# Kernel tuning notes

Hardware: AMD Instinct MI355X
Metric: run time of the kernel (lower is better)

Reference implementation:

```python
import jax, jax.numpy as jnp
import numpy as np

PS = 32
EMBED_DIM = 768
IN_CH = 3
IMG = 1024
NUM_PATCHES = 992  # ini_row = i for H=1024, so need i+32 <= 1024
SPIKE_IDX = np.array([5, 300, 800])
SPIKE_VAL = 1.0e6  # makes val ~= 23.94 < 24 -> nearest size 16 -> subdivided


def _token_layout(iw_np, num_patches, ps, H):
    """Replicates the module's data-dependent patch-size / subpatch-position logic.
    Returns static (rows, cols, sizes) for every output token, in emission order."""
    avg = iw_np.mean()
    val = np.minimum(ps * avg ** 0.05 / iw_np ** 0.05, float(ps))
    choices = np.array([32, 16, 8, 4], dtype=np.float64)  # argmin picks first on tie, like min(list)
    sizes = choices[np.argmin(np.abs(val[:, None] - choices[None, :]), axis=1)].astype(np.int64)
    rows, cols, szs = [], [], []
    for i in range(num_patches):
        ini_col = (i * ps) % H
        ini_row = (i * ps * ps) // H
        s = int(sizes[i])
        if 3 < s < ps:
            ns = ps // s  # num_subpatches; subpatch_size == s
            for j in range(ns):
                rows.append(ini_row + (j * s) // ns)
                cols.append(ini_col + (j * s) % (ns * s))
                szs.append(s)
        else:
            rows.append(ini_row)
            cols.append(ini_col)
            szs.append(ps)
    return np.asarray(rows), np.asarray(cols), np.asarray(szs)


def _embed(x, W, b, rows, cols, szs, ps):
    E, C = W.shape[0], W.shape[1]
    B = x.shape[0]
    T = szs.shape[0]
    out = jnp.zeros((B, T, E), dtype=x.dtype)
    for s in np.unique(szs):
        s = int(s)
        idx = np.nonzero(szs == s)[0]  # static token slots for this size group
        r, c = rows[idx], cols[idx]
        if s == ps:
            Wf = W
        else:
            kd = ps // s  # fold the ps x ps kernel down to s x s, as in the module
            Wf = W.reshape(E, C, kd, kd, s, s).sum(axis=(2, 3))
        ar = np.arange(s)
        # gather [B, C, K, s, s] sub-patches with static advanced indexing
        patches = x[:, :, r[:, None, None] + ar[None, :, None], c[:, None, None] + ar[None, None, :]]
        tok = jnp.einsum('bckhw,echw->bke', patches, Wf) + b  # stride==kernel -> 1 token each
        out = out.at[:, jnp.asarray(idx), :].set(tok)
    return out


def setup_inputs() -> dict:
    key = jax.random.key(0)
    k_x, k_w, k_iw, k_b = jax.random.split(key, 4)
    x = jax.random.normal(k_x, (8, IN_CH, IMG, IMG), dtype=jnp.float32)
    iw = jax.random.uniform(k_iw, (1, NUM_PATCHES), dtype=jnp.float32, minval=0.5, maxval=1.5)
    iw = iw.at[0, SPIKE_IDX].set(SPIKE_VAL)  # 3 high-importance patches -> size-16 subdivision
    W = jax.random.normal(k_w, (EMBED_DIM, IN_CH, PS, PS), dtype=jnp.float32) * 0.02
    b = jax.random.normal(k_b, (EMBED_DIM,), dtype=jnp.float32) * 0.02
    return {"x": x, "importance_weights": iw, "W": W, "b": b, "num_patches": NUM_PATCHES}


def reference(x, importance_weights, W, b, num_patches):
    iw = np.asarray(importance_weights)[0]
    rows, cols, szs = _token_layout(iw, int(num_patches), PS, x.shape[3])
    return _embed(x, W, b, rows, cols, szs, PS)  # [B, T, E]
```

## Files before the change

### kernel.cpp

```cpp
#include <hip/hip_runtime.h>


typedef __attribute__((ext_vector_type(8))) short bf16x8;
typedef __attribute__((ext_vector_type(4))) float f32x4;

#define K_DIM 3072
#define N_DIM 768
#define KSPLIT 2

__device__ __forceinline__ unsigned short f2bf(float f) {
  unsigned int u = __float_as_uint(f);
  u += 0x7fffu + ((u >> 16) & 1u);
  return (unsigned short)(u >> 16);
}

__device__ __forceinline__ void gload16(const void* g, void* l) {
  __builtin_amdgcn_global_load_lds(
      (const __attribute__((address_space(1))) void*)g,
      (__attribute__((address_space(3))) void*)l, 16, 0, 0);
}

__global__ __launch_bounds__(1024)
void prep_kernel(const float* __restrict__ W, unsigned short* __restrict__ Wb, int w4,
                 const float* __restrict__ bias, float* __restrict__ out, int out4,
                 const float* __restrict__ iw, int P,
                 int* __restrict__ tokBase, int* __restrict__ tokMask,
                 int NB_W, int NB_BIAS) {
  int bid = blockIdx.x;
  int tid = threadIdx.x;
  if (bid < NB_W) {
    int idx = bid * 1024 + tid;
    if (idx < w4) {
      float4 f = *(const float4*)(W + (size_t)idx * 4);
      ushort4 o;
      o.x = f2bf(f.x); o.y = f2bf(f.y); o.z = f2bf(f.z); o.w = f2bf(f.w);
      *(ushort4*)(Wb + (size_t)idx * 4) = o;
    }
    return;
  }
  if (bid < NB_W + NB_BIAS) {
    int idx = (bid - NB_W) * 1024 + tid;
    if (idx < out4) {
      int n = (idx % (N_DIM / 4)) * 4;
      *(float4*)(out + (size_t)idx * 4) = *(const float4*)(bias + n);
    }
    return;
  }
  __shared__ double s_wsum[16];
  __shared__ double s_avg;
  __shared__ int s_cnt[1024];
  float v = (tid < P) ? iw[tid] : 0.0f;
  double d = (double)v;
#pragma unroll
  for (int off = 32; off > 0; off >>= 1) d += __shfl_down(d, off, 64);
  if ((tid & 63) == 0) s_wsum[tid >> 6] = d;
  __syncthreads();
  if (tid == 0) {
    double s = 0.0;
    for (int i = 0; i < 16; ++i) s += s_wsum[i];
    s_avg = s / (double)P;
  }
  __syncthreads();
  int cnt = 0, sz = 32;
  if (tid < P) {
    double val = 32.0 * pow(s_avg / (double)v, 0.05);
    if (val > 32.0) val = 32.0;
    sz = (val >= 24.0) ? 32 : (val >= 12.0) ? 16 : (val >= 6.0) ? 8 : 4;
    cnt = (sz < 32) ? (32 / sz) : 1;
  }
  s_cnt[tid] = cnt;
  __syncthreads();
  for (int dl = 1; dl < 1024; dl <<= 1) {
    int add = (tid >= dl) ? s_cnt[tid - dl] : 0;
    __syncthreads();
    s_cnt[tid] += add;
    __syncthreads();
  }
  if (tid < P) {
    int off = s_cnt[tid] - cnt;
    int ini_col = (tid * 32) & 1023;
    int ini_row = (tid * 32 * 32) >> 10;
    if (sz == 32) {
      tokBase[off] = ini_row * 1024 + ini_col;
      tokMask[off] = 31;
    } else {
      int ns = 32 / sz;
      for (int j = 0; j < ns; ++j) {
        int r = ini_row + (j * sz) / ns;
        int c = ini_col + ((j * sz) & 31);
        tokBase[off + j] = r * 1024 + c;
        tokMask[off + j] = sz - 1;
      }
    }
  }
}

__global__ __launch_bounds__(256)
void gather_kernel(const float* __restrict__ x,
                   const int* __restrict__ tokBase,
                   const int* __restrict__ tokMask,
                   unsigned short* __restrict__ Ab) {
  int t = blockIdx.x;
  int b = blockIdx.y;
  int T = gridDim.x;
  int m = b * T + t;
  int base = tokBase[t];
  int mask = tokMask[t];
  int sh = __popc(mask);
  const float* xb = x + (size_t)b * 3145728 + (size_t)base;
  unsigned short* arow = Ab + (size_t)m * K_DIM;
#pragma unroll
  for (int it = 0; it < 3; ++it) {
    int g = it * 256 + threadIdx.x;
    int p = g * 4;
    int c = p >> 10;
    int f = p & 1023;
    int h = (f >> sh) & mask;
    int w = f & mask;
    float4 fv = *(const float4*)(xb + (size_t)c * 1048576 + h * 1024 + w);
    ushort4 o;
    o.x = f2bf(fv.x); o.y = f2bf(fv.y); o.z = f2bf(fv.z); o.w = f2bf(fv.w);
    *(ushort4*)(arow + p) = o;
  }
}

__global__ __launch_bounds__(256, 4)
void gemm_kernel(const unsigned short* __restrict__ A, const unsigned short* __restrict__ Wb,
                 float* __restrict__ out, int Mtot) {
  __shared__ unsigned short Alds[128 * 32];
  __shared__ unsigned short Blds[128 * 32];
  int tid = threadIdx.x;
  int lane = tid & 63;
  int wave = tid >> 6;
  int wr = wave >> 1, wc = wave & 1;
  int mBase = blockIdx.y * 128;
  int nBase = blockIdx.x * 128;
  int kBase = blockIdx.z * (K_DIM / KSPLIT);

  f32x4 acc[4][4] = {};

  int sr = lane >> 2;
  int sc = lane & 3;
  const unsigned short* Ag0 = A + (size_t)(mBase + wave * 32 + sr) * K_DIM + sc * 8 + kBase;
  const unsigned short* Ag1 = Ag0 + (size_t)16 * K_DIM;
  const unsigned short* Bg0 = Wb + (size_t)(nBase + wave * 32 + sr) * K_DIM + sc * 8 + kBase;
  const unsigned short* Bg1 = Bg0 + (size_t)16 * K_DIM;
  unsigned short* Al0 = Alds + wave * 1024 + lane * 8;
  unsigned short* Al1 = Al0 + 512;
  unsigned short* Bl0 = Blds + wave * 1024 + lane * 8;
  unsigned short* Bl1 = Bl0 + 512;

  int rr = lane & 15, q = lane >> 4;

  for (int k0 = 0; k0 < K_DIM / KSPLIT; k0 += 32) {
    gload16(Ag0 + k0, Al0);
    gload16(Ag1 + k0, Al1);
    gload16(Bg0 + k0, Bl0);
    gload16(Bg1 + k0, Bl1);
    __syncthreads();

    bf16x8 aF[4], bF[4];
#pragma unroll
    for (int i = 0; i < 4; ++i)
      aF[i] = *(const bf16x8*)&Alds[(wr * 64 + i * 16 + rr) * 32 + q * 8];
#pragma unroll
    for (int j = 0; j < 4; ++j)
      bF[j] = *(const bf16x8*)&Blds[(wc * 64 + j * 16 + rr) * 32 + q * 8];
#pragma unroll
    for (int i = 0; i < 4; ++i)
#pragma unroll
      for (int j = 0; j < 4; ++j)
        acc[i][j] = __builtin_amdgcn_mfma_f32_16x16x32_bf16(aF[i], bF[j], acc[i][j], 0, 0, 0);
    __syncthreads();
  }

#pragma unroll
  for (int j = 0; j < 4; ++j) {
    int n = nBase + wc * 64 + j * 16 + rr;
#pragma unroll
    for (int i = 0; i < 4; ++i) {
      int mrow = mBase + wr * 64 + i * 16 + q * 4;
#pragma unroll
      for (int r2 = 0; r2 < 4; ++r2) {
        int m = mrow + r2;
        if (m < Mtot) atomicAdd(&out[(size_t)m * N_DIM + n], acc[i][j][r2]);
      }
    }
  }
}

extern "C" void kernel_launch(void* const* d_in, const int* in_sizes, int n_in,
                              void* d_out, int out_size, void* d_ws, size_t ws_size,
                              hipStream_t stream) {
  const float* x  = (const float*)d_in[0];
  const float* iw = (const float*)d_in[1];
  const float* W  = (const float*)d_in[2];
  const float* b  = (const float*)d_in[3];
  int P = in_sizes[1];
  int B = in_sizes[0] / (3 * 1024 * 1024);
  int E = in_sizes[3];
  int T = out_size / (B * E);
  int Mtot = B * T;
  int Mpad = (Mtot + 127) & ~127;

  char* ws = (char*)d_ws;
  int* tokBase = (int*)ws;
  int* tokMask = (int*)(ws + 32768);
  unsigned short* Wb = (unsigned short*)(ws + 65536);
  unsigned short* Ab = (unsigned short*)(ws + 65536 + (size_t)E * K_DIM * 2);

  int w4 = E * K_DIM / 4;
  int out4 = out_size / 4;
  int NB_W = (w4 + 1023) / 1024;
  int NB_BIAS = (out4 + 1023) / 1024;
  prep_kernel<<<NB_W + NB_BIAS + 1, 1024, 0, stream>>>(
      W, Wb, w4, b, (float*)d_out, out4, iw, P, tokBase, tokMask, NB_W, NB_BIAS);

  dim3 gGrid(T, B);
  gather_kernel<<<gGrid, 256, 0, stream>>>(x, tokBase, tokMask, Ab);

  dim3 grid(N_DIM / 128, Mpad / 128, KSPLIT);
  gemm_kernel<<<grid, 256, 0, stream>>>(Ab, Wb, (float*)d_out, Mtot);
}
```

Measured before the change: 262.9 us.

## Drop split-K atomics, fuse bias into GEMM epilogue, register-prefetch pipeline

Removes the split-K decomposition, so each GEMM block covers the full K range and writes its results directly with the bias added, rather than pre-filling the output with bias and accumulating with atomics. The global_load_lds path is replaced by register prefetching: the next K-slice is loaded into registers while the current slice is staged into LDS and fed to MFMA. This removes the bias-fill pass and the atomic traffic, at the cost of half as many GEMM blocks, which lowers parallelism. The launch bound is relaxed to allow more registers for the prefetch buffers.

```diff
diff --git a/kernel.cpp b/kernel.cpp
--- a/kernel.cpp
+++ b/kernel.cpp
@@ -6,7 +6,6 @@
 
 #define K_DIM 3072
 #define N_DIM 768
-#define KSPLIT 2
 
 __device__ __forceinline__ unsigned short f2bf(float f) {
   unsigned int u = __float_as_uint(f);
@@ -14,18 +13,10 @@
   return (unsigned short)(u >> 16);
 }
 
-__device__ __forceinline__ void gload16(const void* g, void* l) {
-  __builtin_amdgcn_global_load_lds(
-      (const __attribute__((address_space(1))) void*)g,
-      (__attribute__((address_space(3))) void*)l, 16, 0, 0);
-}
-
 __global__ __launch_bounds__(1024)
 void prep_kernel(const float* __restrict__ W, unsigned short* __restrict__ Wb, int w4,
-                 const float* __restrict__ bias, float* __restrict__ out, int out4,
                  const float* __restrict__ iw, int P,
-                 int* __restrict__ tokBase, int* __restrict__ tokMask,
-                 int NB_W, int NB_BIAS) {
+                 int* __restrict__ tokBase, int* __restrict__ tokMask, int NB_W) {
   int bid = blockIdx.x;
   int tid = threadIdx.x;
   if (bid < NB_W) {
@@ -35,14 +26,6 @@
       ushort4 o;
       o.x = f2bf(f.x); o.y = f2bf(f.y); o.z = f2bf(f.z); o.w = f2bf(f.w);
       *(ushort4*)(Wb + (size_t)idx * 4) = o;
-    }
-    return;
-  }
-  if (bid < NB_W + NB_BIAS) {
-    int idx = (bid - NB_W) * 1024 + tid;
-    if (idx < out4) {
-      int n = (idx % (N_DIM / 4)) * 4;
-      *(float4*)(out + (size_t)idx * 4) = *(const float4*)(bias + n);
     }
     return;
   }
@@ -124,9 +107,9 @@
   }
 }
 
-__global__ __launch_bounds__(256, 4)
+__global__ __launch_bounds__(256, 2)
 void gemm_kernel(const unsigned short* __restrict__ A, const unsigned short* __restrict__ Wb,
-                 float* __restrict__ out, int Mtot) {
+                 const float* __restrict__ bias, float* __restrict__ out, int Mtot) {
   __shared__ unsigned short Alds[128 * 32];
   __shared__ unsigned short Blds[128 * 32];
   int tid = threadIdx.x;
@@ -135,55 +118,76 @@
   int wr = wave >> 1, wc = wave & 1;
   int mBase = blockIdx.y * 128;
   int nBase = blockIdx.x * 128;
-  int kBase = blockIdx.z * (K_DIM / KSPLIT);
 
   f32x4 acc[4][4] = {};
 
-  int sr = lane >> 2;
-  int sc = lane & 3;
-  const unsigned short* Ag0 = A + (size_t)(mBase + wave * 32 + sr) * K_DIM + sc * 8 + kBase;
-  const unsigned short* Ag1 = Ag0 + (size_t)16 * K_DIM;
-  const unsigned short* Bg0 = Wb + (size_t)(nBase + wave * 32 + sr) * K_DIM + sc * 8 + kBase;
-  const unsigned short* Bg1 = Bg0 + (size_t)16 * K_DIM;
-  unsigned short* Al0 = Alds + wave * 1024 + lane * 8;
-  unsigned short* Al1 = Al0 + 512;
-  unsigned short* Bl0 = Blds + wave * 1024 + lane * 8;
-  unsigned short* Bl1 = Bl0 + 512;
+  const unsigned short* Ag0 = A + (size_t)(mBase + (tid >> 2)) * K_DIM + (tid & 3) * 8;
+  const unsigned short* Ag1 = Ag0 + (size_t)64 * K_DIM;
+  const unsigned short* Bg0 = Wb + (size_t)(nBase + (tid >> 2)) * K_DIM + (tid & 3) * 8;
+  const unsigned short* Bg1 = Bg0 + (size_t)64 * K_DIM;
+  unsigned short* Al0 = Alds + tid * 8;
+  unsigned short* Al1 = Al0 + 2048;
+  unsigned short* Bl0 = Blds + tid * 8;
+  unsigned short* Bl1 = Bl0 + 2048;
 
   int rr = lane & 15, q = lane >> 4;
 
-  for (int k0 = 0; k0 < K_DIM / KSPLIT; k0 += 32) {
-    gload16(Ag0 + k0, Al0);
-    gload16(Ag1 + k0, Al1);
-    gload16(Bg0 + k0, Bl0);
-    gload16(Bg1 + k0, Bl1);
-    __syncthreads();
-
-    bf16x8 aF[4], bF[4];
-#pragma unroll
-    for (int i = 0; i < 4; ++i)
-      aF[i] = *(const bf16x8*)&Alds[(wr * 64 + i * 16 + rr) * 32 + q * 8];
-#pragma unroll
-    for (int j = 0; j < 4; ++j)
-      bF[j] = *(const bf16x8*)&Blds[(wc * 64 + j * 16 + rr) * 32 + q * 8];
-#pragma unroll
-    for (int i = 0; i < 4; ++i)
-#pragma unroll
-      for (int j = 0; j < 4; ++j)
-        acc[i][j] = __builtin_amdgcn_mfma_f32_16x16x32_bf16(aF[i], bF[j], acc[i][j], 0, 0, 0);
-    __syncthreads();
+  int4 ra0, ra1, rb0, rb1;
+  int4 sa0, sa1, sb0, sb1;
+
+  ra0 = *(const int4*)(Ag0); ra1 = *(const int4*)(Ag1);
+  rb0 = *(const int4*)(Bg0); rb1 = *(const int4*)(Bg1);
+
+#define MFMA_STAGE()                                                        \
+  {                                                                         \
+    bf16x8 aF[4], bF[4];                                                    \
+    _Pragma("unroll")                                                       \
+    for (int i = 0; i < 4; ++i)                                             \
+      aF[i] = *(const bf16x8*)&Alds[(wr * 64 + i * 16 + rr) * 32 + q * 8];  \
+    _Pragma("unroll")                                                       \
+    for (int j = 0; j < 4; ++j)                                             \
+      bF[j] = *(const bf16x8*)&Blds[(wc * 64 + j * 16 + rr) * 32 + q * 8];  \
+    _Pragma("unroll")                                                       \
+    for (int i = 0; i < 4; ++i)                                             \
+      _Pragma("unroll")                                                     \
+      for (int j = 0; j < 4; ++j)                                           \
+        acc[i][j] = __builtin_amdgcn_mfma_f32_16x16x32_bf16(aF[i], bF[j],   \
+                                                            acc[i][j], 0, 0, 0); \
+  }
+
+  for (int k0 = 0; k0 < K_DIM; k0 += 64) {
+    if (k0 + 32 < K_DIM) {
+      sa0 = *(const int4*)(Ag0 + k0 + 32); sa1 = *(const int4*)(Ag1 + k0 + 32);
+      sb0 = *(const int4*)(Bg0 + k0 + 32); sb1 = *(const int4*)(Bg1 + k0 + 32);
+    }
+    __syncthreads();
+    *(int4*)Al0 = ra0; *(int4*)Al1 = ra1;
+    *(int4*)Bl0 = rb0; *(int4*)Bl1 = rb1;
+    __syncthreads();
+    MFMA_STAGE();
+
+    if (k0 + 64 < K_DIM) {
+      ra0 = *(const int4*)(Ag0 + k0 + 64); ra1 = *(const int4*)(Ag1 + k0 + 64);
+      rb0 = *(const int4*)(Bg0 + k0 + 64); rb1 = *(const int4*)(Bg1 + k0 + 64);
+    }
+    __syncthreads();
+    *(int4*)Al0 = sa0; *(int4*)Al1 = sa1;
+    *(int4*)Bl0 = sb0; *(int4*)Bl1 = sb1;
+    __syncthreads();
+    MFMA_STAGE();
   }
 
 #pragma unroll
   for (int j = 0; j < 4; ++j) {
     int n = nBase + wc * 64 + j * 16 + rr;
+    float bv = bias[n];
 #pragma unroll
     for (int i = 0; i < 4; ++i) {
       int mrow = mBase + wr * 64 + i * 16 + q * 4;
 #pragma unroll
       for (int r2 = 0; r2 < 4; ++r2) {
         int m = mrow + r2;
-        if (m < Mtot) atomicAdd(&out[(size_t)m * N_DIM + n], acc[i][j][r2]);
+        if (m < Mtot) out[(size_t)m * N_DIM + n] = acc[i][j][r2] + bv;
       }
     }
   }
@@ -210,15 +214,12 @@
   unsigned short* Ab = (unsigned short*)(ws + 65536 + (size_t)E * K_DIM * 2);
 
   int w4 = E * K_DIM / 4;
-  int out4 = out_size / 4;
   int NB_W = (w4 + 1023) / 1024;
-  int NB_BIAS = (out4 + 1023) / 1024;
-  prep_kernel<<<NB_W + NB_BIAS + 1, 1024, 0, stream>>>(
-      W, Wb, w4, b, (float*)d_out, out4, iw, P, tokBase, tokMask, NB_W, NB_BIAS);
+  prep_kernel<<<NB_W + 1, 1024, 0, stream>>>(W, Wb, w4, iw, P, tokBase, tokMask, NB_W);
 
   dim3 gGrid(T, B);
   gather_kernel<<<gGrid, 256, 0, stream>>>(x, tokBase, tokMask, Ab);
 
-  dim3 grid(N_DIM / 128, Mpad / 128, KSPLIT);
-  gemm_kernel<<<grid, 256, 0, stream>>>(Ab, Wb, (float*)d_out, Mtot);
-}
+  dim3 grid(N_DIM / 128, Mpad / 128);
+  gemm_kernel<<<grid, 256, 0, stream>>>(Ab, Wb, b, (float*)d_out, Mtot);
+}
```

After: 262.2 us. No clear change (-0.3%).
